# Kernel optimization log

Hardware: AMD Instinct MI355X
Metric: run time of the kernel (lower is better)

Reference implementation:

```python
import jax, jax.numpy as jnp
import numpy as np

# Fixed mock-config geometry
B, S, H = 8, 4096, 2048
NK, NV, DK, DV = 2, 2, 4, 4
KDIM = NK * DK          # 8
VDIM = NV * DV          # 8
CONV_DIM = 2 * KDIM + VDIM  # 24
KSZ = 4                 # causal conv kernel size
EPS = 1e-6


def setup_inputs() -> dict:
    key = jax.random.key(0)
    ks = jax.random.split(key, 7)
    scaled = lambda k, shape, fan: jax.random.normal(k, shape, jnp.float32) * (1.0 / np.sqrt(fan))
    return {
        "x": jax.random.normal(ks[0], (B, S, H), jnp.float32),
        "w_qkv": scaled(ks[1], (CONV_DIM, H), H),   # in_proj_qkv.weight
        "w_z": scaled(ks[2], (VDIM, H), H),         # in_proj_z.weight
        "w_b": scaled(ks[3], (NV, H), H),           # in_proj_b.weight
        "w_a": scaled(ks[4], (NV, H), H),           # in_proj_a.weight
        "w_out": scaled(ks[5], (H, VDIM), VDIM),    # out_proj.weight
        "conv_w": jax.random.normal(ks[6], (CONV_DIM, 1, KSZ), jnp.float32) * 0.5,  # depthwise conv weight
        "dt_bias": jnp.ones((NV,), jnp.float32),
        "A_log": jnp.log(jnp.linspace(1.0, 2.0, NV)).astype(jnp.float32),
        "norm_w": jnp.ones((DV,), jnp.float32),     # MockRMSNormGated weight
    }


def reference(x, w_qkv, w_z, w_b, w_a, w_out, conv_w, dt_bias, A_log, norm_w):
    b_, s_, _ = x.shape
    # qkv projection -> [B, C, S] for depthwise causal conv
    mixed = jnp.einsum('bsh,ch->bcs', x, w_qkv)
    # torch conv1d(padding=K-1) then [:, :, :S] == causal left-pad K-1
    conv = jax.lax.conv_general_dilated(
        mixed, conv_w, window_strides=(1,), padding=[(KSZ - 1, 0)],
        dimension_numbers=('NCH', 'OIH', 'NCH'), feature_group_count=CONV_DIM)
    mixed = jax.nn.silu(conv).transpose(0, 2, 1)  # [B, S, C]

    z = jnp.einsum('bsh,vh->bsv', x, w_z).reshape(b_, s_, NV, DV)
    bb = jnp.einsum('bsh,nh->bsn', x, w_b)  # [B, S, NV]
    aa = jnp.einsum('bsh,nh->bsn', x, w_a)  # [B, S, NV]

    query = mixed[..., :KDIM].reshape(b_, s_, NK, DK)
    key_ = mixed[..., KDIM:2 * KDIM].reshape(b_, s_, NK, DK)
    value = mixed[..., 2 * KDIM:].reshape(b_, s_, NV, DV)

    beta = jax.nn.sigmoid(bb)                                    # [B, S, NV]
    g = -jnp.exp(A_log) * jax.nn.softplus(aa + dt_bias)          # [B, S, NV], fp32
    # num_v_heads // num_k_heads == 1 -> no repeat_interleave

    # mock chunk_gated_delta_rule: value + beta * (q + k) + g
    core = value + beta[..., None] * (query + key_) + g[..., None]  # [B, S, NV, DV]

    # gated RMSNorm over head_v_dim (fp32 math)
    h = core.astype(jnp.float32)
    var = jnp.mean(h * h, axis=-1, keepdims=True)
    h = h * jax.lax.rsqrt(var + EPS) * norm_w
    h = h * jax.nn.silu(z.astype(jnp.float32))

    out = jnp.einsum('bsv,hv->bsh', h.reshape(b_, s_, VDIM), w_out)
    return out
```

## Files before the change

### kernel.cpp

```cpp
#include <hip/hip_runtime.h>
#include <hip/hip_bf16.h>
#include <math.h>
#include <cstddef>

#define BB    8
#define SS    4096
#define HH    2048
#define ROWS  (BB*SS)
#define NC    36
#define NCP   40
#define KC    64
#define XSTR  65

#define MIX_OFF 131072

__global__ __launch_bounds__(256) void pack_wt(
    const float* __restrict__ w_qkv, const float* __restrict__ w_z,
    const float* __restrict__ w_b,   const float* __restrict__ w_a,
    float* __restrict__ wt) {
  int idx = blockIdx.x * 256 + threadIdx.x;
  if (idx >= HH * NCP) return;
  int k = idx / NCP, c = idx - (idx / NCP) * NCP;
  float v = 0.f;
  if      (c < 24) v = w_qkv[c * HH + k];
  else if (c < 32) v = w_z[(c - 24) * HH + k];
  else if (c < 34) v = w_b[(c - 32) * HH + k];
  else if (c < 36) v = w_a[(c - 34) * HH + k];
  wt[idx] = v;
}

__global__ __launch_bounds__(256, 2) void proj36(
    const float* __restrict__ x, const float* __restrict__ wt,
    float* __restrict__ mix) {
  __shared__ float sm[4 * 64 * XSTR];
  const int tid  = threadIdx.x;
  const int lane = tid & 63;
  const int wv   = __builtin_amdgcn_readfirstlane(tid >> 6);
  const int r0   = blockIdx.x * 64;

  float* xs = sm + wv * 64 * XSTR;
  float acc[NC];
#pragma unroll
  for (int c = 0; c < NC; ++c) acc[c] = 0.f;

  const int kbase0 = wv * 512;
  const int srow = lane >> 4;
  const int scol = (lane & 15) * 4;
  const float* xg = x + (size_t)r0 * HH + kbase0 + scol;

  float4 buf[16];
#pragma unroll
  for (int p = 0; p < 16; ++p)
    buf[p] = *(const float4*)(xg + (size_t)(p * 4 + srow) * HH);

  for (int ch = 0; ch < 8; ++ch) {
#pragma unroll
    for (int p = 0; p < 16; ++p) {
      float* dst = xs + (p * 4 + srow) * XSTR + scol;
      dst[0] = buf[p].x; dst[1] = buf[p].y; dst[2] = buf[p].z; dst[3] = buf[p].w;
    }
    if (ch < 7) {
      const float* xg2 = xg + (ch + 1) * KC;
#pragma unroll
      for (int p = 0; p < 16; ++p)
        buf[p] = *(const float4*)(xg2 + (size_t)(p * 4 + srow) * HH);
    }
    const float* wrow = wt + (size_t)(kbase0 + ch * KC) * NCP;
    const float* xr = xs + lane * XSTR;
#pragma unroll 2
    for (int k = 0; k < KC; ++k) {
      float xv = xr[k];
#pragma unroll
      for (int c = 0; c < NC; ++c)
        acc[c] = fmaf(wrow[k * NCP + c], xv, acc[c]);
    }
  }

  __syncthreads();
#pragma unroll
  for (int c = 0; c < NC; ++c) sm[tid * 37 + c] = acc[c];
  __syncthreads();
  for (int i = 0; i < 9; ++i) {
    int idx = i * 256 + tid;
    int row = idx / NC, c = idx - row * NC;
    float s = sm[row * 37 + c] + sm[(64 + row) * 37 + c]
            + sm[(128 + row) * 37 + c] + sm[(192 + row) * 37 + c];
    mix[(size_t)r0 * NC + idx] = s;
  }
}

__global__ __launch_bounds__(256) void fuse_out(
    const float* __restrict__ mix,  const float* __restrict__ conv_w,
    const float* __restrict__ dt_bias, const float* __restrict__ A_log,
    const float* __restrict__ norm_w,  const float* __restrict__ w_out,
    float* __restrict__ out) {
  __shared__ float m36[67 * 37];
  __shared__ float hb[64 * 8];
  const int tid = threadIdx.x;
  const int r0  = blockIdx.x * 64;

  const long base = (long)(r0 - 3) * NC;
  for (int idx = tid; idx < 67 * NC; idx += 256) {
    int row = idx / NC, c = idx - row * NC;
    long g = base + idx;
    m36[row * 37 + c] = (g >= 0) ? mix[g] : 0.f;
  }
  __syncthreads();

  if (tid < 128) {
    const int row  = tid >> 1, n = tid & 1;
    const int spos = (r0 + row) & (SS - 1);
    float cv[12];
#pragma unroll
    for (int j = 0; j < 12; ++j) {
      int c = (j >> 2) * 8 + n * 4 + (j & 3);
      float s = 0.f;
#pragma unroll
      for (int k = 0; k < 4; ++k)
        if (spos + k - 3 >= 0) s += m36[(row + k) * 37 + c] * conv_w[c * 4 + k];
      cv[j] = s / (1.f + __expf(-s));
    }
    float bbv  = m36[(row + 3) * 37 + 32 + n];
    float aav  = m36[(row + 3) * 37 + 34 + n];
    float beta = 1.f / (1.f + __expf(-bbv));
    float spin = aav + dt_bias[n];
    float sp   = (spin > 20.f) ? spin : __logf(1.f + __expf(spin));
    float g    = -__expf(A_log[n]) * sp;
    float core[4], var = 0.f;
#pragma unroll
    for (int d = 0; d < 4; ++d) {
      core[d] = cv[8 + d] + beta * (cv[d] + cv[4 + d]) + g;
      var += core[d] * core[d];
    }
    float rs = rsqrtf(var * 0.25f + 1e-6f);
#pragma unroll
    for (int d = 0; d < 4; ++d) {
      float z = m36[(row + 3) * 37 + 24 + n * 4 + d];
      hb[row * 8 + n * 4 + d] =
          core[d] * rs * norm_w[d] * (z / (1.f + __expf(-z)));
    }
  }
  __syncthreads();

  const int c0a = tid * 4, c0b = 1024 + tid * 4;
  float4 wr[16];
#pragma unroll
  for (int i = 0; i < 4; ++i) {
    wr[i * 2]     = *(const float4*)(w_out + (size_t)(c0a + i) * 8);
    wr[i * 2 + 1] = *(const float4*)(w_out + (size_t)(c0a + i) * 8 + 4);
    wr[8 + i * 2]     = *(const float4*)(w_out + (size_t)(c0b + i) * 8);
    wr[8 + i * 2 + 1] = *(const float4*)(w_out + (size_t)(c0b + i) * 8 + 4);
  }
  for (int row = 0; row < 64; ++row) {
    float h[8];
#pragma unroll
    for (int v = 0; v < 8; ++v) h[v] = hb[row * 8 + v];
    float4 oa, ob;
#pragma unroll
    for (int i = 0; i < 4; ++i) {
      const float4 wa0 = wr[i * 2], wa1 = wr[i * 2 + 1];
      const float4 wb0 = wr[8 + i * 2], wb1 = wr[8 + i * 2 + 1];
      (&oa.x)[i] = h[0]*wa0.x + h[1]*wa0.y + h[2]*wa0.z + h[3]*wa0.w
                 + h[4]*wa1.x + h[5]*wa1.y + h[6]*wa1.z + h[7]*wa1.w;
      (&ob.x)[i] = h[0]*wb0.x + h[1]*wb0.y + h[2]*wb0.z + h[3]*wb0.w
                 + h[4]*wb1.x + h[5]*wb1.y + h[6]*wb1.z + h[7]*wb1.w;
    }
    float* op = out + (size_t)(r0 + row) * HH;
    *(float4*)(op + c0a) = oa;
    *(float4*)(op + c0b) = ob;
  }
}

extern "C" void kernel_launch(void* const* d_in, const int* in_sizes, int n_in,
                              void* d_out, int out_size, void* d_ws, size_t ws_size,
                              hipStream_t stream) {
  (void)in_sizes; (void)n_in; (void)out_size; (void)ws_size;
  const float* x      = (const float*)d_in[0];
  const float* w_qkv  = (const float*)d_in[1];
  const float* w_z    = (const float*)d_in[2];
  const float* w_b    = (const float*)d_in[3];
  const float* w_a    = (const float*)d_in[4];
  const float* w_out  = (const float*)d_in[5];
  const float* conv_w = (const float*)d_in[6];
  const float* dt_b   = (const float*)d_in[7];
  const float* A_log  = (const float*)d_in[8];
  const float* norm_w = (const float*)d_in[9];
  float* out = (float*)d_out;
  float* ws  = (float*)d_ws;
  float* wt  = ws;
  float* mix = ws + MIX_OFF;

  pack_wt<<<dim3((HH * NCP + 255) / 256), dim3(256), 0, stream>>>(
      w_qkv, w_z, w_b, w_a, wt);
  proj36<<<dim3(ROWS / 64), dim3(256), 0, stream>>>(x, wt, mix);
  fuse_out<<<dim3(ROWS / 64), dim3(256), 0, stream>>>(
      mix, conv_w, dt_b, A_log, norm_w, w_out, out);
}
```

Before: 573.2 us.

## Split K across eight waves in projection, halve output tile, use nontemporal stores

The projection kernel moves from 4 to 8 waves per block. Each wave now covers a 256-wide K slice in 32-column chunks, and a two-pass shared-memory reduction sums the eight partial accumulators under the larger shared footprint. The aim is more waves in flight to hide latency on the memory-bound x stream. The output kernel processes 32 rows per block instead of 64, doubling the grid, and writes its results with nontemporal stores to avoid polluting the cache. In exchange, the new code adds reduction and synchronisation overhead and makes each fetch chunk smaller.

New measurement: 499.8 us. 12.8% less time.

```diff
diff --git a/kernel.cpp b/kernel.cpp
--- a/kernel.cpp
+++ b/kernel.cpp
@@ -1,5 +1,4 @@
 #include <hip/hip_runtime.h>
-#include <hip/hip_bf16.h>
 #include <math.h>
 #include <cstddef>
 
@@ -9,8 +8,11 @@
 #define ROWS  (BB*SS)
 #define NC    36
 #define NCP   40
-#define KC    64
-#define XSTR  65
+#define KC    32
+#define XST   33
+#define KSL   256
+
+typedef float vfloat4 __attribute__((ext_vector_type(4)));
 
 #define MIX_OFF 131072
 
@@ -29,44 +31,44 @@
   wt[idx] = v;
 }
 
-__global__ __launch_bounds__(256, 2) void proj36(
+__global__ __launch_bounds__(512, 4) void proj36(
     const float* __restrict__ x, const float* __restrict__ wt,
     float* __restrict__ mix) {
-  __shared__ float sm[4 * 64 * XSTR];
+  __shared__ float sm[8 * 64 * XST];
   const int tid  = threadIdx.x;
   const int lane = tid & 63;
   const int wv   = __builtin_amdgcn_readfirstlane(tid >> 6);
   const int r0   = blockIdx.x * 64;
 
-  float* xs = sm + wv * 64 * XSTR;
+  float* xs = sm + wv * 64 * XST;
   float acc[NC];
 #pragma unroll
   for (int c = 0; c < NC; ++c) acc[c] = 0.f;
 
-  const int kbase0 = wv * 512;
-  const int srow = lane >> 4;
-  const int scol = (lane & 15) * 4;
+  const int kbase0 = wv * KSL;
+  const int srow = lane >> 3;
+  const int scol = (lane & 7) * 4;
   const float* xg = x + (size_t)r0 * HH + kbase0 + scol;
 
-  float4 buf[16];
-#pragma unroll
-  for (int p = 0; p < 16; ++p)
-    buf[p] = *(const float4*)(xg + (size_t)(p * 4 + srow) * HH);
+  float4 buf[8];
+#pragma unroll
+  for (int p = 0; p < 8; ++p)
+    buf[p] = *(const float4*)(xg + (size_t)(p * 8 + srow) * HH);
 
   for (int ch = 0; ch < 8; ++ch) {
 #pragma unroll
-    for (int p = 0; p < 16; ++p) {
-      float* dst = xs + (p * 4 + srow) * XSTR + scol;
+    for (int p = 0; p < 8; ++p) {
+      float* dst = xs + (p * 8 + srow) * XST + scol;
       dst[0] = buf[p].x; dst[1] = buf[p].y; dst[2] = buf[p].z; dst[3] = buf[p].w;
     }
     if (ch < 7) {
       const float* xg2 = xg + (ch + 1) * KC;
 #pragma unroll
-      for (int p = 0; p < 16; ++p)
-        buf[p] = *(const float4*)(xg2 + (size_t)(p * 4 + srow) * HH);
+      for (int p = 0; p < 8; ++p)
+        buf[p] = *(const float4*)(xg2 + (size_t)(p * 8 + srow) * HH);
     }
     const float* wrow = wt + (size_t)(kbase0 + ch * KC) * NCP;
-    const float* xr = xs + lane * XSTR;
+    const float* xr = xs + lane * XST;
 #pragma unroll 2
     for (int k = 0; k < KC; ++k) {
       float xv = xr[k];
@@ -77,15 +79,23 @@
   }
 
   __syncthreads();
-#pragma unroll
-  for (int c = 0; c < NC; ++c) sm[tid * 37 + c] = acc[c];
-  __syncthreads();
-  for (int i = 0; i < 9; ++i) {
-    int idx = i * 256 + tid;
-    int row = idx / NC, c = idx - row * NC;
-    float s = sm[row * 37 + c] + sm[(64 + row) * 37 + c]
-            + sm[(128 + row) * 37 + c] + sm[(192 + row) * 37 + c];
-    mix[(size_t)r0 * NC + idx] = s;
+  const int myhalf = lane >> 5;
+  const int rr = lane & 31;
+  for (int half = 0; half < 2; ++half) {
+    if (half) __syncthreads();
+    if (myhalf == half) {
+#pragma unroll
+      for (int c = 0; c < NC; ++c)
+        sm[(wv * 32 + rr) * 37 + c] = acc[c];
+    }
+    __syncthreads();
+    for (int idx = tid; idx < 32 * NC; idx += 512) {
+      int row = idx / NC;
+      float s = 0.f;
+#pragma unroll
+      for (int w = 0; w < 8; ++w) s += sm[(w * 32 + row) * 37 + (idx - row * NC)];
+      mix[(size_t)(r0 + half * 32) * NC + idx] = s;
+    }
   }
 }
 
@@ -94,20 +104,20 @@
     const float* __restrict__ dt_bias, const float* __restrict__ A_log,
     const float* __restrict__ norm_w,  const float* __restrict__ w_out,
     float* __restrict__ out) {
-  __shared__ float m36[67 * 37];
-  __shared__ float hb[64 * 8];
+  __shared__ float m36[35 * 37];
+  __shared__ float hb[32 * 8];
   const int tid = threadIdx.x;
-  const int r0  = blockIdx.x * 64;
+  const int r0  = blockIdx.x * 32;
 
   const long base = (long)(r0 - 3) * NC;
-  for (int idx = tid; idx < 67 * NC; idx += 256) {
+  for (int idx = tid; idx < 35 * NC; idx += 256) {
     int row = idx / NC, c = idx - row * NC;
     long g = base + idx;
     m36[row * 37 + c] = (g >= 0) ? mix[g] : 0.f;
   }
   __syncthreads();
 
-  if (tid < 128) {
+  if (tid < 64) {
     const int row  = tid >> 1, n = tid & 1;
     const int spos = (r0 + row) & (SS - 1);
     float cv[12];
@@ -151,23 +161,23 @@
     wr[8 + i * 2]     = *(const float4*)(w_out + (size_t)(c0b + i) * 8);
     wr[8 + i * 2 + 1] = *(const float4*)(w_out + (size_t)(c0b + i) * 8 + 4);
   }
-  for (int row = 0; row < 64; ++row) {
+  for (int row = 0; row < 32; ++row) {
     float h[8];
 #pragma unroll
     for (int v = 0; v < 8; ++v) h[v] = hb[row * 8 + v];
-    float4 oa, ob;
+    vfloat4 oa, ob;
 #pragma unroll
     for (int i = 0; i < 4; ++i) {
       const float4 wa0 = wr[i * 2], wa1 = wr[i * 2 + 1];
       const float4 wb0 = wr[8 + i * 2], wb1 = wr[8 + i * 2 + 1];
-      (&oa.x)[i] = h[0]*wa0.x + h[1]*wa0.y + h[2]*wa0.z + h[3]*wa0.w
-                 + h[4]*wa1.x + h[5]*wa1.y + h[6]*wa1.z + h[7]*wa1.w;
-      (&ob.x)[i] = h[0]*wb0.x + h[1]*wb0.y + h[2]*wb0.z + h[3]*wb0.w
-                 + h[4]*wb1.x + h[5]*wb1.y + h[6]*wb1.z + h[7]*wb1.w;
+      oa[i] = h[0]*wa0.x + h[1]*wa0.y + h[2]*wa0.z + h[3]*wa0.w
+            + h[4]*wa1.x + h[5]*wa1.y + h[6]*wa1.z + h[7]*wa1.w;
+      ob[i] = h[0]*wb0.x + h[1]*wb0.y + h[2]*wb0.z + h[3]*wb0.w
+            + h[4]*wb1.x + h[5]*wb1.y + h[6]*wb1.z + h[7]*wb1.w;
     }
     float* op = out + (size_t)(r0 + row) * HH;
-    *(float4*)(op + c0a) = oa;
-    *(float4*)(op + c0b) = ob;
+    __builtin_nontemporal_store(oa, (vfloat4*)(op + c0a));
+    __builtin_nontemporal_store(ob, (vfloat4*)(op + c0b));
   }
 }
 
@@ -192,7 +202,7 @@
 
   pack_wt<<<dim3((HH * NCP + 255) / 256), dim3(256), 0, stream>>>(
       w_qkv, w_z, w_b, w_a, wt);
-  proj36<<<dim3(ROWS / 64), dim3(256), 0, stream>>>(x, wt, mix);
-  fuse_out<<<dim3(ROWS / 64), dim3(256), 0, stream>>>(
+  proj36<<<dim3(ROWS / 64), dim3(512), 0, stream>>>(x, wt, mix);
+  fuse_out<<<dim3(ROWS / 32), dim3(256), 0, stream>>>(
       mix, conv_w, dt_b, A_log, norm_w, w_out, out);
 }
```
